# Kernel optimization log

Hardware: AMD Instinct MI355X
Metric: run time of the kernel (lower is better)

Reference implementation:

```python
import jax, jax.numpy as jnp
import numpy as np

B = 8; H = 128; W = 128; C = 256
NH = 16; HD = 16          # head_dim hard-coded to 16 in source
WS = 8; SS = 4            # window size / shift size
HID = 1024                # mlp hidden = 4 * C
SCALE = HD ** (-0.5)


def _rel_pos_index(ws):
    # same construction as torch buffer relative_position_index
    coords = np.stack(np.meshgrid(np.arange(ws), np.arange(ws), indexing='ij')).reshape(2, -1)
    rel = (coords[:, :, None] - coords[:, None, :]).transpose(1, 2, 0).copy()
    rel[..., 0] += ws - 1
    rel[..., 1] += ws - 1
    rel[..., 0] *= 2 * ws - 1
    return rel.sum(-1)  # (N, N) ints


def _attn_mask(h, w, ws, ss):
    # shifted-window mask, matches calculate_mask()
    img = np.zeros((h, w))
    sl = (slice(0, -ws), slice(-ws, -ss), slice(-ss, None))
    c = 0
    for hs in sl:
        for wsl in sl:
            img[hs, wsl] = c
            c += 1
    mw = img.reshape(h // ws, ws, w // ws, ws).transpose(0, 2, 1, 3).reshape(-1, ws * ws)
    d = mw[:, None, :] - mw[:, :, None]  # (nW, N, N)
    return np.where(d == 0, 0.0, -100.0).astype(np.float32)


def _ln(x, g, b, eps=1e-5):
    m = x.mean(-1, keepdims=True)
    v = ((x - m) ** 2).mean(-1, keepdims=True)
    return (x - m) * jax.lax.rsqrt(v + eps) * g + b


def setup_inputs() -> dict:
    key = jax.random.key(0)
    ks = jax.random.split(key, 12)
    inner = NH * HD
    std = 0.02
    return {
        'x': jax.random.normal(ks[0], (B, H * W, C), jnp.float32),
        'ln1_g': jnp.ones((C,), jnp.float32),
        'ln1_b': jnp.zeros((C,), jnp.float32),
        'q_w': jax.random.normal(ks[1], (C, inner), jnp.float32) * std,
        'q_b': jnp.zeros((inner,), jnp.float32),
        'k_w': jax.random.normal(ks[2], (C, inner), jnp.float32) * std,
        'k_b': jnp.zeros((inner,), jnp.float32),
        'v_w': jax.random.normal(ks[3], (C, inner), jnp.float32) * std,
        'v_b': jnp.zeros((inner,), jnp.float32),
        'rpb': jax.random.normal(ks[4], ((2 * WS - 1) * (2 * WS - 1), NH), jnp.float32) * std,
        'proj_w': jax.random.normal(ks[5], (inner, C), jnp.float32) * std,
        'proj_b': jnp.zeros((C,), jnp.float32),
        'ln2_g': jnp.ones((C,), jnp.float32),
        'ln2_b': jnp.zeros((C,), jnp.float32),
        'fc1_w': jax.random.normal(ks[6], (C, HID), jnp.float32) * std,
        'fc1_b': jnp.zeros((HID,), jnp.float32),
        'fc2_w': jax.random.normal(ks[7], (HID, C), jnp.float32) * std,
        'fc2_b': jnp.zeros((C,), jnp.float32),
        'H_in': 128,
        'W_in': 128,
    }


def reference(x, ln1_g, ln1_b, q_w, q_b, k_w, k_b, v_w, v_b, rpb,
              proj_w, proj_b, ln2_g, ln2_b, fc1_w, fc1_b, fc2_w, fc2_b,
              H_in, W_in):
    N = WS * WS
    nW = (H // WS) * (W // WS)
    idx = _rel_pos_index(WS)                       # static int (N, N)
    mask = jnp.asarray(_attn_mask(H, W, WS, SS))   # (nW, N, N)

    shortcut = x
    h = _ln(x, ln1_g, ln1_b).reshape(B, H, W, C)
    h = jnp.roll(h, (-SS, -SS), axis=(1, 2))
    # window partition -> (B*nW, N, C)
    h = h.reshape(B, H // WS, WS, W // WS, WS, C).transpose(0, 1, 3, 2, 4, 5)
    h = h.reshape(B * nW, N, C)

    q = (h @ q_w + q_b).reshape(-1, N, NH, HD).transpose(0, 2, 1, 3) * SCALE
    k = (h @ k_w + k_b).reshape(-1, N, NH, HD).transpose(0, 2, 1, 3)
    v = (h @ v_w + v_b).reshape(-1, N, NH, HD).transpose(0, 2, 1, 3)

    attn = jnp.einsum('bhnd,bhmd->bhnm', q, k)     # (B*nW, NH, N, N)
    bias = rpb[idx.reshape(-1)].reshape(N, N, NH).transpose(2, 0, 1)
    attn = attn + bias[None]
    attn = attn.reshape(B, nW, NH, N, N) + mask[None, :, None]
    attn = jax.nn.softmax(attn.reshape(B * nW, NH, N, N), axis=-1)

    o = jnp.einsum('bhnm,bhmd->bhnd', attn, v)
    o = o.transpose(0, 2, 1, 3).reshape(B * nW, N, NH * HD)
    o = o @ proj_w + proj_b

    # window reverse + roll back
    o = o.reshape(B, H // WS, W // WS, WS, WS, C).transpose(0, 1, 3, 2, 4, 5)
    o = o.reshape(B, H, W, C)
    o = jnp.roll(o, (SS, SS), axis=(1, 2)).reshape(B, H * W, C)

    x = shortcut + o
    h2 = _ln(x, ln2_g, ln2_b)
    h2 = jax.nn.gelu(h2 @ fc1_w + fc1_b, approximate=False)
    return x + (h2 @ fc2_w + fc2_b)
```

## Files before the change

### kernel.cpp

```cpp
#include <hip/hip_runtime.h>
#include <hip/hip_bf16.h>
#include <stdint.h>


#define SLOT ((size_t)64 << 20)

typedef __attribute__((ext_vector_type(8))) short bf16x8;
typedef __attribute__((ext_vector_type(4))) float f32x4;

union FU { float f; unsigned u; };

__device__ inline float bflo(unsigned p) { FU x; x.u = p << 16; return x.f; }
__device__ inline float bfhi(unsigned p) { FU x; x.u = p & 0xffff0000u; return x.f; }
__device__ inline unsigned short f2bf(float f) {
  FU x; x.f = f;
  unsigned r = x.u + 0x7fff + ((x.u >> 16) & 1);
  return (unsigned short)(r >> 16);
}
__device__ inline unsigned packbf2(float a, float b) {
  FU x, y; x.f = a; y.f = b;
  unsigned ra = (x.u + 0x7fff + ((x.u >> 16) & 1)) >> 16;
  unsigned rb = (y.u + 0x7fff + ((y.u >> 16) & 1)) & 0xffff0000u;
  return ra | rb;
}

__device__ inline float fast_gelu(float v) {
  return v / (1.0f + __expf(-1.702f * v));
}

__device__ inline void gload16(const void* g, void* l) {
  __builtin_amdgcn_global_load_lds(
      (const __attribute__((address_space(1))) unsigned int*)g,
      (__attribute__((address_space(3))) unsigned int*)l, 16, 0, 0);
}


__global__ __launch_bounds__(256) void build_qkvw(
    const float* __restrict__ qw, const float* __restrict__ kw, const float* __restrict__ vw,
    const float* __restrict__ qb, const float* __restrict__ kb, const float* __restrict__ vb,
    unsigned short* __restrict__ wt, float* __restrict__ bias) {
  int i = blockIdx.x * 256 + threadIdx.x;
  if (i < 768 * 256) {
    int n = i >> 8, c = i & 255;
    const float* w = (n < 256) ? qw : (n < 512 ? kw : vw);
    const float sc = (n < 256) ? 0.25f : 1.0f;
    int nn = n & 255;
    wt[i] = f2bf(sc * w[c * 256 + nn]);
  }
  if (i < 768) {
    bias[i] = (i < 256) ? 0.25f * qb[i] : (i < 512 ? kb[i - 256] : vb[i - 512]);
  }
}

__global__ __launch_bounds__(256) void wconv_t(
    const float* __restrict__ src, unsigned short* __restrict__ dst, int R, int C) {
  int i = blockIdx.x * 256 + threadIdx.x;
  if (i >= R * C) return;
  int n = i / R, c = i - n * R;
  dst[i] = f2bf(src[(size_t)c * C + n]);
}

__global__ __launch_bounds__(256) void ln1_roll_win(
    const float* __restrict__ x, const float* __restrict__ g, const float* __restrict__ b,
    unsigned short* __restrict__ hwin) {
  const int tok = blockIdx.x * 4 + (threadIdx.x >> 6);
  const int l = threadIdx.x & 63;
  const int n = tok & 63, wi = (tok >> 6) & 255, bb = tok >> 14;
  const int wh = wi >> 4, ww = wi & 15, r = n >> 3, c = n & 7;
  const int hs = (wh * 8 + r + 4) & 127;
  const int wsx = (ww * 8 + c + 4) & 127;
  const float* xr = x + ((size_t)bb * 16384 + hs * 128 + wsx) * 256;
  float4 v = *(const float4*)(xr + l * 4);
  float s = v.x + v.y + v.z + v.w;
#pragma unroll
  for (int off = 32; off; off >>= 1) s += __shfl_xor(s, off);
  const float mean = s * (1.f / 256.f);
  const float d0 = v.x - mean, d1 = v.y - mean, d2 = v.z - mean, d3 = v.w - mean;
  float vv = d0 * d0 + d1 * d1 + d2 * d2 + d3 * d3;
#pragma unroll
  for (int off = 32; off; off >>= 1) vv += __shfl_xor(vv, off);
  const float rs = rsqrtf(vv * (1.f / 256.f) + 1e-5f);
  float4 gg = *(const float4*)(g + l * 4);
  float4 bv = *(const float4*)(b + l * 4);
  uint2 outv;
  outv.x = packbf2(d0 * rs * gg.x + bv.x, d1 * rs * gg.y + bv.y);
  outv.y = packbf2(d2 * rs * gg.z + bv.z, d3 * rs * gg.w + bv.w);
  *(uint2*)(hwin + (size_t)tok * 256 + l * 4) = outv;
}

template <int EPI, int K, int N, int NBX>
__global__ __launch_bounds__(256) void gemm128(
    const unsigned short* __restrict__ A, const unsigned short* __restrict__ Bt,
    const float* __restrict__ bias, unsigned short* __restrict__ Cb,
    float* __restrict__ Cf) {
  __shared__ __align__(16) unsigned short smem[2][2][128 * 64];
  const int nwg = gridDim.x;
  const int q = nwg >> 3;
  const int swz = (blockIdx.x & 7) * q + (blockIdx.x >> 3);
  const int m0 = (swz / NBX) * 128;
  const int n0 = (swz % NBX) * 128;

  const int t = threadIdx.x, w = t >> 6, l = t & 63;
  const int lg = l >> 4, lm = l & 15;
  const int wr = w >> 1, wc = w & 1;

  const int srow = w * 32 + (l >> 3);
  const int scol = ((l & 7) ^ (l >> 3)) * 8;
  const unsigned short* Ap = A + (size_t)(m0 + srow) * K + scol;
  const unsigned short* Bp = Bt + (size_t)(n0 + srow) * K + scol;

  const int cb = n0 + wc * 64 + lm;
  f32x4 acc[4][4];
#pragma unroll
  for (int n = 0; n < 4; ++n) {
    const float bv = bias[cb + n * 16];
#pragma unroll
    for (int m = 0; m < 4; ++m) acc[m][n] = (f32x4){bv, bv, bv, bv};
  }

  constexpr int NT = K >> 6;
  const int cx = lg ^ (lm & 7);

#pragma unroll
  for (int i = 0; i < 4; ++i) {
    gload16(Ap + (size_t)(i * 8) * K, &smem[0][0][(w * 32 + i * 8) * 64]);
    gload16(Bp + (size_t)(i * 8) * K, &smem[0][1][(w * 32 + i * 8) * 64]);
  }
  __syncthreads();

#pragma unroll
  for (int kt = 0; kt < NT; ++kt) {
    const int cur = kt & 1;
    if (kt + 1 < NT) {
      const int ko = (kt + 1) << 6;
#pragma unroll
      for (int i = 0; i < 4; ++i) {
        gload16(Ap + (size_t)(i * 8) * K + ko, &smem[cur ^ 1][0][(w * 32 + i * 8) * 64]);
        gload16(Bp + (size_t)(i * 8) * K + ko, &smem[cur ^ 1][1][(w * 32 + i * 8) * 64]);
      }
    }
#pragma unroll
    for (int kk = 0; kk < 64; kk += 32) {
      const int ch = (cx ^ (kk >> 3)) * 8;
      bf16x8 af[4], bfr[4];
#pragma unroll
      for (int m = 0; m < 4; ++m)
        af[m] = *(const bf16x8*)&smem[cur][0][(wr * 64 + m * 16 + lm) * 64 + ch];
#pragma unroll
      for (int n = 0; n < 4; ++n)
        bfr[n] = *(const bf16x8*)&smem[cur][1][(wc * 64 + n * 16 + lm) * 64 + ch];
#pragma unroll
      for (int m = 0; m < 4; ++m)
#pragma unroll
        for (int n = 0; n < 4; ++n)
          acc[m][n] = __builtin_amdgcn_mfma_f32_16x16x32_bf16(af[m], bfr[n], acc[m][n], 0, 0, 0);
    }
    if (kt + 1 < NT) __syncthreads();
  }

  __syncthreads();
  float* Lp = (float*)smem;
#pragma unroll
  for (int m = 0; m < 4; ++m) {
#pragma unroll
    for (int n = 0; n < 4; ++n) {
      const int col = wc * 64 + n * 16 + lm;
#pragma unroll
      for (int r = 0; r < 4; ++r) {
        const int row = wr * 64 + m * 16 + lg * 4 + r;
        Lp[row * 128 + (col ^ (lg << 4))] = acc[m][n][r];
      }
    }
  }
  __syncthreads();
  const int rr0 = w * 32 + (l >> 5);
  const int cg = (l & 31) * 4;
#pragma unroll
  for (int p = 0; p < 16; ++p) {
    const int row = rr0 + p * 2;
    const int sc = cg ^ (((row >> 2) & 3) << 4);
    float4 v = *(const float4*)&Lp[row * 128 + sc];
    if (EPI == 2) {
      v.x = fast_gelu(v.x); v.y = fast_gelu(v.y);
      v.z = fast_gelu(v.z); v.w = fast_gelu(v.w);
    }
    if (EPI == 3) {
      float4* op = (float4*)&Cf[(size_t)(m0 + row) * N + n0 + cg];
      float4 o = *op;
      o.x += v.x; o.y += v.y; o.z += v.z; o.w += v.w;
      *op = o;
    } else {
      uint2 pk;
      pk.x = packbf2(v.x, v.y);
      pk.y = packbf2(v.z, v.w);
      *(uint2*)&Cb[(size_t)(m0 + row) * N + n0 + cg] = pk;
    }
  }
}

__global__ __launch_bounds__(256) void attn_mfma(
    const unsigned short* __restrict__ qkv, const float* __restrict__ rpb,
    unsigned short* __restrict__ o) {
  __shared__ float rps[16][226];
  __shared__ __align__(16) unsigned short Pl[4][64][72];
  const int win = blockIdx.x;
  const int wh = (win >> 4) & 15, ww = win & 15;
  const int t = threadIdx.x, wv = t >> 6, l = t & 63;
  const int lg = l >> 4, lm = l & 15;
  const unsigned short* base = qkv + (size_t)win * 64 * 768;

  for (int i = t; i < 3600; i += 256) rps[i & 15][i >> 4] = rpb[i];
  __syncthreads();

  const bool eH = (wh == 15), eW = (ww == 15);
  const bool edge = eH || eW;

  int qv[4], liq[4];
#pragma unroll
  for (int nt = 0; nt < 4; ++nt) {
    const int qn = nt * 16 + lm, ri = qn >> 3, ci = qn & 7;
    qv[nt] = ri * 15 + ci;
    liq[nt] = (eH ? (ri < 4 ? 1 : 2) : 0) * 3 + (eW ? (ci < 4 ? 1 : 2) : 0);
  }
  int kv[4][4], ljk[4][4];
#pragma unroll
  for (int mt = 0; mt < 4; ++mt)
#pragma unroll
    for (int r = 0; r < 4; ++r) {
      const int kn = mt * 16 + 4 * lg + r, rj = kn >> 3, cj = kn & 7;
      kv[mt][r] = rj * 15 + cj;
      ljk[mt][r] = (eH ? (rj < 4 ? 1 : 2) : 0) * 3 + (eW ? (cj < 4 ? 1 : 2) : 0);
    }

  const bf16x8 zf = {0, 0, 0, 0, 0, 0, 0, 0};

#pragma unroll 1
  for (int hi = 0; hi < 4; ++hi) {
    const int h = wv * 4 + hi;
    bf16x8 kf[4], qf[4];
#pragma unroll
    for (int i = 0; i < 4; ++i) {
      kf[i] = (lg < 2)
          ? *(const bf16x8*)(base + (size_t)(i * 16 + lm) * 768 + 256 + h * 16 + lg * 8)
          : zf;
      qf[i] = (lg < 2)
          ? *(const bf16x8*)(base + (size_t)(i * 16 + lm) * 768 + h * 16 + lg * 8)
          : zf;
    }
    f32x4 acc[4][4];
#pragma unroll
    for (int mt = 0; mt < 4; ++mt)
#pragma unroll
      for (int nt = 0; nt < 4; ++nt)
        acc[mt][nt] = (f32x4){0.f, 0.f, 0.f, 0.f};
#pragma unroll
    for (int mt = 0; mt < 4; ++mt)
#pragma unroll
      for (int nt = 0; nt < 4; ++nt)
        acc[mt][nt] = __builtin_amdgcn_mfma_f32_16x16x32_bf16(kf[mt], qf[nt], acc[mt][nt], 0, 0, 0);

#pragma unroll
    for (int nt = 0; nt < 4; ++nt) {
      float mx = -1e30f;
#pragma unroll
      for (int mt = 0; mt < 4; ++mt)
#pragma unroll
        for (int r = 0; r < 4; ++r) {
          float s = acc[mt][nt][r] + rps[h][qv[nt] - kv[mt][r] + 112];
          if (edge) s += (liq[nt] == ljk[mt][r]) ? 0.f : -100.f;
          acc[mt][nt][r] = s;
          mx = fmaxf(mx, s);
        }
      mx = fmaxf(mx, __shfl_xor(mx, 16));
      mx = fmaxf(mx, __shfl_xor(mx, 32));
      float sum = 0.f;
#pragma unroll
      for (int mt = 0; mt < 4; ++mt)
#pragma unroll
        for (int r = 0; r < 4; ++r) {
          const float p = __expf(acc[mt][nt][r] - mx);
          acc[mt][nt][r] = p;
          sum += p;
        }
      sum += __shfl_xor(sum, 16);
      sum += __shfl_xor(sum, 32);
      const float inv = 1.f / sum;
      const int qn = nt * 16 + lm;
#pragma unroll
      for (int mt = 0; mt < 4; ++mt) {
        uint2 pk;
        pk.x = packbf2(acc[mt][nt][0] * inv, acc[mt][nt][1] * inv);
        pk.y = packbf2(acc[mt][nt][2] * inv, acc[mt][nt][3] * inv);
        *(uint2*)&Pl[wv][qn][mt * 16 + 4 * lg] = pk;
      }
    }

    f32x4 oacc[4];
#pragma unroll
    for (int mt = 0; mt < 4; ++mt) oacc[mt] = (f32x4){0.f, 0.f, 0.f, 0.f};
#pragma unroll
    for (int kk = 0; kk < 2; ++kk) {
      bf16x8 vf;
#pragma unroll
      for (int j = 0; j < 8; ++j)
        vf[j] = (short)base[(size_t)(kk * 32 + lg * 8 + j) * 768 + 512 + h * 16 + lm];
#pragma unroll
      for (int mt = 0; mt < 4; ++mt) {
        bf16x8 pf = *(const bf16x8*)&Pl[wv][mt * 16 + lm][kk * 32 + lg * 8];
        oacc[mt] = __builtin_amdgcn_mfma_f32_16x16x32_bf16(pf, vf, oacc[mt], 0, 0, 0);
      }
    }
#pragma unroll
    for (int mt = 0; mt < 4; ++mt)
#pragma unroll
      for (int r = 0; r < 4; ++r)
        o[((size_t)win * 64 + mt * 16 + 4 * lg + r) * 256 + h * 16 + lm] = f2bf(oacc[mt][r]);
  }
}

__global__ __launch_bounds__(256) void scatter_ln2(
    const float* __restrict__ x, const unsigned short* __restrict__ po,
    const float* __restrict__ g, const float* __restrict__ b,
    float* __restrict__ x2, unsigned short* __restrict__ h2) {
  const int tok = blockIdx.x * 4 + (threadIdx.x >> 6);
  const int l = threadIdx.x & 63;
  const int bb = tok >> 14, pix = tok & 16383, hy = pix >> 7, wx = pix & 127;
  const int hr = (hy + 124) & 127, wc = (wx + 124) & 127;
  const int src = ((bb << 8) + (hr >> 3) * 16 + (wc >> 3)) * 64 + (hr & 7) * 8 + (wc & 7);
  float4 xv = *(const float4*)(x + (size_t)tok * 256 + l * 4);
  uint2 pv = *(const uint2*)(po + (size_t)src * 256 + l * 4);
  const float y0 = xv.x + bflo(pv.x);
  const float y1 = xv.y + bfhi(pv.x);
  const float y2 = xv.z + bflo(pv.y);
  const float y3 = xv.w + bfhi(pv.y);
  *(float4*)(x2 + (size_t)tok * 256 + l * 4) = make_float4(y0, y1, y2, y3);
  float s = y0 + y1 + y2 + y3;
#pragma unroll
  for (int off = 32; off; off >>= 1) s += __shfl_xor(s, off);
  const float mean = s * (1.f / 256.f);
  const float d0 = y0 - mean, d1 = y1 - mean, d2 = y2 - mean, d3 = y3 - mean;
  float vv = d0 * d0 + d1 * d1 + d2 * d2 + d3 * d3;
#pragma unroll
  for (int off = 32; off; off >>= 1) vv += __shfl_xor(vv, off);
  const float rs = rsqrtf(vv * (1.f / 256.f) + 1e-5f);
  float4 gg = *(const float4*)(g + l * 4);
  float4 bv = *(const float4*)(b + l * 4);
  uint2 outv;
  outv.x = packbf2(d0 * rs * gg.x + bv.x, d1 * rs * gg.y + bv.y);
  outv.y = packbf2(d2 * rs * gg.z + bv.z, d3 * rs * gg.w + bv.w);
  *(uint2*)(h2 + (size_t)tok * 256 + l * 4) = outv;
}


extern "C" void kernel_launch(void* const* d_in, const int* in_sizes, int n_in,
                              void* d_out, int out_size, void* d_ws, size_t ws_size,
                              hipStream_t stream) {
  const float* x = (const float*)d_in[0];
  const float* ln1g = (const float*)d_in[1];
  const float* ln1b = (const float*)d_in[2];
  const float* qw = (const float*)d_in[3];
  const float* qb = (const float*)d_in[4];
  const float* kw = (const float*)d_in[5];
  const float* kb = (const float*)d_in[6];
  const float* vw = (const float*)d_in[7];
  const float* vb = (const float*)d_in[8];
  const float* rpb = (const float*)d_in[9];
  const float* pw = (const float*)d_in[10];
  const float* pb = (const float*)d_in[11];
  const float* ln2g = (const float*)d_in[12];
  const float* ln2b = (const float*)d_in[13];
  const float* f1w = (const float*)d_in[14];
  const float* f1b = (const float*)d_in[15];
  const float* f2w = (const float*)d_in[16];
  const float* f2b = (const float*)d_in[17];
  float* out = (float*)d_out;

  char* wsb = (char*)d_ws;
  unsigned short* hwin = (unsigned short*)(wsb);
  unsigned short* qkv = (unsigned short*)(wsb + SLOT);
  unsigned short* po = (unsigned short*)(wsb + 4 * SLOT);
  unsigned short* g1 = qkv;
  unsigned short* wqkvt = (unsigned short*)(wsb + 5 * SLOT);
  unsigned short* projt = wqkvt + 768 * 256;
  unsigned short* fc1t = projt + 256 * 256;
  unsigned short* fc2t = fc1t + 1024 * 256;
  float* bqkv = (float*)(fc2t + 256 * 1024);

  build_qkvw<<<768, 256, 0, stream>>>(qw, kw, vw, qb, kb, vb, wqkvt, bqkv);
  wconv_t<<<256, 256, 0, stream>>>(pw, projt, 256, 256);
  wconv_t<<<1024, 256, 0, stream>>>(f1w, fc1t, 256, 1024);
  wconv_t<<<1024, 256, 0, stream>>>(f2w, fc2t, 1024, 256);

  ln1_roll_win<<<32768, 256, 0, stream>>>(x, ln1g, ln1b, hwin);
  gemm128<0, 256, 768, 6><<<6 * 1024, 256, 0, stream>>>(hwin, wqkvt, bqkv, qkv, nullptr);
  attn_mfma<<<2048, 256, 0, stream>>>(qkv, rpb, hwin);
  gemm128<0, 256, 256, 2><<<2 * 1024, 256, 0, stream>>>(hwin, projt, pb, po, nullptr);
  scatter_ln2<<<32768, 256, 0, stream>>>(x, po, ln2g, ln2b, out, hwin);
  gemm128<2, 256, 1024, 8><<<8 * 1024, 256, 0, stream>>>(hwin, fc1t, f1b, g1, nullptr);
  gemm128<3, 1024, 256, 2><<<2 * 1024, 256, 0, stream>>>(g1, fc2t, f2b, nullptr, out);
}
```

Before: 688.1 us.

## Fuse MLP fc1, GELU and fc2 into a single kernel keeping hidden tile in LDS

```diff
diff --git a/kernel.cpp b/kernel.cpp
--- a/kernel.cpp
+++ b/kernel.cpp
@@ -180,21 +180,134 @@
     const int row = rr0 + p * 2;
     const int sc = cg ^ (((row >> 2) & 3) << 4);
     float4 v = *(const float4*)&Lp[row * 128 + sc];
-    if (EPI == 2) {
-      v.x = fast_gelu(v.x); v.y = fast_gelu(v.y);
-      v.z = fast_gelu(v.z); v.w = fast_gelu(v.w);
-    }
-    if (EPI == 3) {
-      float4* op = (float4*)&Cf[(size_t)(m0 + row) * N + n0 + cg];
-      float4 o = *op;
-      o.x += v.x; o.y += v.y; o.z += v.z; o.w += v.w;
-      *op = o;
-    } else {
-      uint2 pk;
-      pk.x = packbf2(v.x, v.y);
-      pk.y = packbf2(v.z, v.w);
-      *(uint2*)&Cb[(size_t)(m0 + row) * N + n0 + cg] = pk;
-    }
+    uint2 pk;
+    pk.x = packbf2(v.x, v.y);
+    pk.y = packbf2(v.z, v.w);
+    *(uint2*)&Cb[(size_t)(m0 + row) * N + n0 + cg] = pk;
+  }
+}
+
+__global__ __launch_bounds__(256, 2) void fused_mlp(
+    const unsigned short* __restrict__ h2, const unsigned short* __restrict__ w1t,
+    const float* __restrict__ b1, const unsigned short* __restrict__ w2t,
+    const float* __restrict__ b2, float* __restrict__ out) {
+  __shared__ __align__(16) unsigned short smem[2 * 64 * 256];
+  unsigned short* As = smem;
+  unsigned short* Hs = smem + 64 * 256;
+  const int nwg = gridDim.x;
+  const int q = nwg >> 3;
+  const int swz = (blockIdx.x & 7) * q + (blockIdx.x >> 3);
+  const int m0 = swz * 64;
+
+  const int t = threadIdx.x, w = t >> 6, l = t & 63;
+  const int lg = l >> 4, lm = l & 15;
+
+#pragma unroll
+  for (int i = 0; i < 8; ++i) {
+    const int row = w * 16 + i * 2 + (l >> 5);
+    const int c = (l & 31) ^ (row & 7);
+    gload16(h2 + (size_t)(m0 + row) * 256 + c * 8, &As[(w * 16 + i * 2) * 256]);
+  }
+
+  f32x4 oacc[4][4];
+#pragma unroll
+  for (int n = 0; n < 4; ++n) {
+    const float bv = b2[w * 64 + n * 16 + lm];
+#pragma unroll
+    for (int m = 0; m < 4; ++m) oacc[m][n] = (f32x4){bv, bv, bv, bv};
+  }
+  __syncthreads();
+
+  for (int hc = 0; hc < 4; ++hc) {
+    if (hc) __syncthreads();
+#pragma unroll
+    for (int half = 0; half < 2; ++half) {
+      f32x4 a1[4][2];
+#pragma unroll
+      for (int n = 0; n < 2; ++n) {
+        const float bv = b1[hc * 256 + w * 64 + half * 32 + n * 16 + lm];
+#pragma unroll
+        for (int m = 0; m < 4; ++m) a1[m][n] = (f32x4){bv, bv, bv, bv};
+      }
+#pragma unroll
+      for (int kk = 0; kk < 8; ++kk) {
+        bf16x8 af[4], bw[2];
+#pragma unroll
+        for (int m = 0; m < 4; ++m) {
+          const int row = m * 16 + lm;
+          af[m] = *(const bf16x8*)((const char*)As + row * 512 +
+                                   ((kk * 64 + lg * 16) ^ ((row & 7) << 4)));
+        }
+#pragma unroll
+        for (int n = 0; n < 2; ++n)
+          bw[n] = *(const bf16x8*)(w1t +
+                   (size_t)(hc * 256 + w * 64 + half * 32 + n * 16 + lm) * 256 +
+                   kk * 32 + lg * 8);
+#pragma unroll
+        for (int m = 0; m < 4; ++m)
+#pragma unroll
+          for (int n = 0; n < 2; ++n)
+            a1[m][n] = __builtin_amdgcn_mfma_f32_16x16x32_bf16(af[m], bw[n], a1[m][n], 0, 0, 0);
+      }
+#pragma unroll
+      for (int m = 0; m < 4; ++m)
+#pragma unroll
+        for (int n = 0; n < 2; ++n)
+#pragma unroll
+          for (int r = 0; r < 4; ++r) {
+            const int hrow = m * 16 + lg * 4 + r;
+            const int hcol = w * 64 + half * 32 + n * 16 + lm;
+            *(unsigned short*)((char*)Hs + hrow * 512 +
+                               ((hcol * 2) ^ ((hrow & 7) << 4))) = f2bf(fast_gelu(a1[m][n][r]));
+          }
+    }
+    __syncthreads();
+#pragma unroll
+    for (int ks = 0; ks < 8; ++ks) {
+      bf16x8 hf[4], bw2[4];
+#pragma unroll
+      for (int m = 0; m < 4; ++m) {
+        const int row = m * 16 + lm;
+        hf[m] = *(const bf16x8*)((const char*)Hs + row * 512 +
+                                 ((ks * 64 + lg * 16) ^ ((row & 7) << 4)));
+      }
+#pragma unroll
+      for (int n = 0; n < 4; ++n)
+        bw2[n] = *(const bf16x8*)(w2t + (size_t)(w * 64 + n * 16 + lm) * 1024 +
+                                  hc * 256 + ks * 32 + lg * 8);
+#pragma unroll
+      for (int m = 0; m < 4; ++m)
+#pragma unroll
+        for (int n = 0; n < 4; ++n)
+          oacc[m][n] = __builtin_amdgcn_mfma_f32_16x16x32_bf16(hf[m], bw2[n], oacc[m][n], 0, 0, 0);
+    }
+  }
+
+  __syncthreads();
+  float* Lf = (float*)smem;
+#pragma unroll
+  for (int m = 0; m < 4; ++m)
+#pragma unroll
+    for (int n = 0; n < 4; ++n) {
+      const int col = w * 64 + n * 16 + lm;
+#pragma unroll
+      for (int r = 0; r < 4; ++r) {
+        const int row = m * 16 + lg * 4 + r;
+        Lf[row * 256 + (col ^ (lg << 4))] = oacc[m][n][r];
+      }
+    }
+  __syncthreads();
+#pragma unroll
+  for (int p = 0; p < 16; ++p) {
+    const int fidx = p * 256 + t;
+    const int row = fidx >> 6;
+    const int c4 = (fidx & 63) * 4;
+    const int c4r = c4 ^ (((row >> 2) & 3) << 4);
+    float4 v = *(const float4*)&Lf[row * 256 + c4r];
+    float4* op = (float4*)&out[(size_t)(m0 + row) * 256 + c4];
+    float4 o = *op;
+    o.x += v.x; o.y += v.y; o.z += v.z; o.w += v.w;
+    *op = o;
   }
 }
 
@@ -379,7 +492,6 @@
   unsigned short* hwin = (unsigned short*)(wsb);
   unsigned short* qkv = (unsigned short*)(wsb + SLOT);
   unsigned short* po = (unsigned short*)(wsb + 4 * SLOT);
-  unsigned short* g1 = qkv;
   unsigned short* wqkvt = (unsigned short*)(wsb + 5 * SLOT);
   unsigned short* projt = wqkvt + 768 * 256;
   unsigned short* fc1t = projt + 256 * 256;
@@ -396,6 +508,5 @@
   attn_mfma<<<2048, 256, 0, stream>>>(qkv, rpb, hwin);
   gemm128<0, 256, 256, 2><<<2 * 1024, 256, 0, stream>>>(hwin, projt, pb, po, nullptr);
   scatter_ln2<<<32768, 256, 0, stream>>>(x, po, ln2g, ln2b, out, hwin);
-  gemm128<2, 256, 1024, 8><<<8 * 1024, 256, 0, stream>>>(hwin, fc1t, f1b, g1, nullptr);
-  gemm128<3, 1024, 256, 2><<<2 * 1024, 256, 0, stream>>>(g1, fc2t, f2b, nullptr, out);
-}
+  fused_mlp<<<2048, 256, 0, stream>>>(hwin, fc1t, f1b, fc2t, f2b, out);
+}
```

Measured after the change: 695.2 us. Within noise of the previous version (+1.0%).

## Halve GEMM K-tile to 32 and split epilogue staging into two halves

Applied to the files above, without the earlier changes.

```diff
diff --git a/kernel.cpp b/kernel.cpp
--- a/kernel.cpp
+++ b/kernel.cpp
@@ -93,7 +93,7 @@
     const unsigned short* __restrict__ A, const unsigned short* __restrict__ Bt,
     const float* __restrict__ bias, unsigned short* __restrict__ Cb,
     float* __restrict__ Cf) {
-  __shared__ __align__(16) unsigned short smem[2][2][128 * 64];
+  __shared__ __align__(16) unsigned short smem[2][2][128 * 32];
   const int nwg = gridDim.x;
   const int q = nwg >> 3;
   const int swz = (blockIdx.x & 7) * q + (blockIdx.x >> 3);
@@ -104,27 +104,27 @@
   const int lg = l >> 4, lm = l & 15;
   const int wr = w >> 1, wc = w & 1;
 
-  const int srow = w * 32 + (l >> 3);
-  const int scol = ((l & 7) ^ (l >> 3)) * 8;
+  const int srow = w * 32 + (l >> 2);
+  const int scol = ((l & 3) ^ ((l >> 2) & 3)) * 8;
   const unsigned short* Ap = A + (size_t)(m0 + srow) * K + scol;
   const unsigned short* Bp = Bt + (size_t)(n0 + srow) * K + scol;
 
-  const int cb = n0 + wc * 64 + lm;
+  const int cbs = n0 + wc * 64 + lm;
   f32x4 acc[4][4];
 #pragma unroll
   for (int n = 0; n < 4; ++n) {
-    const float bv = bias[cb + n * 16];
+    const float bv = bias[cbs + n * 16];
 #pragma unroll
     for (int m = 0; m < 4; ++m) acc[m][n] = (f32x4){bv, bv, bv, bv};
   }
 
-  constexpr int NT = K >> 6;
-  const int cx = lg ^ (lm & 7);
-
-#pragma unroll
-  for (int i = 0; i < 4; ++i) {
-    gload16(Ap + (size_t)(i * 8) * K, &smem[0][0][(w * 32 + i * 8) * 64]);
-    gload16(Bp + (size_t)(i * 8) * K, &smem[0][1][(w * 32 + i * 8) * 64]);
+  constexpr int NT = K >> 5;
+  const int chA = (lg ^ (lm & 3)) * 8;
+
+#pragma unroll
+  for (int i = 0; i < 2; ++i) {
+    gload16(Ap + (size_t)(i * 16) * K, &smem[0][0][(w * 32 + i * 16) * 32]);
+    gload16(Bp + (size_t)(i * 16) * K, &smem[0][1][(w * 32 + i * 16) * 32]);
   }
   __syncthreads();
 
@@ -132,68 +132,69 @@
   for (int kt = 0; kt < NT; ++kt) {
     const int cur = kt & 1;
     if (kt + 1 < NT) {
-      const int ko = (kt + 1) << 6;
-#pragma unroll
-      for (int i = 0; i < 4; ++i) {
-        gload16(Ap + (size_t)(i * 8) * K + ko, &smem[cur ^ 1][0][(w * 32 + i * 8) * 64]);
-        gload16(Bp + (size_t)(i * 8) * K + ko, &smem[cur ^ 1][1][(w * 32 + i * 8) * 64]);
+      const int ko = (kt + 1) << 5;
+#pragma unroll
+      for (int i = 0; i < 2; ++i) {
+        gload16(Ap + (size_t)(i * 16) * K + ko, &smem[cur ^ 1][0][(w * 32 + i * 16) * 32]);
+        gload16(Bp + (size_t)(i * 16) * K + ko, &smem[cur ^ 1][1][(w * 32 + i * 16) * 32]);
       }
     }
-#pragma unroll
-    for (int kk = 0; kk < 64; kk += 32) {
-      const int ch = (cx ^ (kk >> 3)) * 8;
-      bf16x8 af[4], bfr[4];
+    bf16x8 af[4], bfr[4];
+#pragma unroll
+    for (int m = 0; m < 4; ++m)
+      af[m] = *(const bf16x8*)&smem[cur][0][(wr * 64 + m * 16 + lm) * 32 + chA];
+#pragma unroll
+    for (int n = 0; n < 4; ++n)
+      bfr[n] = *(const bf16x8*)&smem[cur][1][(wc * 64 + n * 16 + lm) * 32 + chA];
+#pragma unroll
+    for (int m = 0; m < 4; ++m)
+#pragma unroll
+      for (int n = 0; n < 4; ++n)
+        acc[m][n] = __builtin_amdgcn_mfma_f32_16x16x32_bf16(af[m], bfr[n], acc[m][n], 0, 0, 0);
+    if (kt + 1 < NT) __syncthreads();
+  }
+
+  float* Lp = (float*)smem;
+#pragma unroll
+  for (int h = 0; h < 2; ++h) {
+    __syncthreads();
+    if (wr == h) {
 #pragma unroll
       for (int m = 0; m < 4; ++m)
-        af[m] = *(const bf16x8*)&smem[cur][0][(wr * 64 + m * 16 + lm) * 64 + ch];
-#pragma unroll
-      for (int n = 0; n < 4; ++n)
-        bfr[n] = *(const bf16x8*)&smem[cur][1][(wc * 64 + n * 16 + lm) * 64 + ch];
-#pragma unroll
-      for (int m = 0; m < 4; ++m)
-#pragma unroll
-        for (int n = 0; n < 4; ++n)
-          acc[m][n] = __builtin_amdgcn_mfma_f32_16x16x32_bf16(af[m], bfr[n], acc[m][n], 0, 0, 0);
-    }
-    if (kt + 1 < NT) __syncthreads();
-  }
-
-  __syncthreads();
-  float* Lp = (float*)smem;
-#pragma unroll
-  for (int m = 0; m < 4; ++m) {
-#pragma unroll
-    for (int n = 0; n < 4; ++n) {
-      const int col = wc * 64 + n * 16 + lm;
-#pragma unroll
-      for (int r = 0; r < 4; ++r) {
-        const int row = wr * 64 + m * 16 + lg * 4 + r;
-        Lp[row * 128 + (col ^ (lg << 4))] = acc[m][n][r];
+#pragma unroll
+        for (int n = 0; n < 4; ++n) {
+          const int col = wc * 64 + n * 16 + lm;
+#pragma unroll
+          for (int r = 0; r < 4; ++r) {
+            const int rowl = m * 16 + lg * 4 + r;
+            Lp[rowl * 128 + (col ^ (lg << 4))] = acc[m][n][r];
+          }
+        }
+    }
+    __syncthreads();
+#pragma unroll
+    for (int p = 0; p < 8; ++p) {
+      const int fidx = p * 256 + t;
+      const int rowl = fidx >> 5;
+      const int c4 = (fidx & 31) * 4;
+      const int sc = c4 ^ (((rowl >> 2) & 3) << 4);
+      float4 v = *(const float4*)&Lp[rowl * 128 + sc];
+      const int grow = m0 + h * 64 + rowl;
+      if (EPI == 2) {
+        v.x = fast_gelu(v.x); v.y = fast_gelu(v.y);
+        v.z = fast_gelu(v.z); v.w = fast_gelu(v.w);
       }
-    }
-  }
-  __syncthreads();
-  const int rr0 = w * 32 + (l >> 5);
-  const int cg = (l & 31) * 4;
-#pragma unroll
-  for (int p = 0; p < 16; ++p) {
-    const int row = rr0 + p * 2;
-    const int sc = cg ^ (((row >> 2) & 3) << 4);
-    float4 v = *(const float4*)&Lp[row * 128 + sc];
-    if (EPI == 2) {
-      v.x = fast_gelu(v.x); v.y = fast_gelu(v.y);
-      v.z = fast_gelu(v.z); v.w = fast_gelu(v.w);
-    }
-    if (EPI == 3) {
-      float4* op = (float4*)&Cf[(size_t)(m0 + row) * N + n0 + cg];
-      float4 o = *op;
-      o.x += v.x; o.y += v.y; o.z += v.z; o.w += v.w;
-      *op = o;
-    } else {
-      uint2 pk;
-      pk.x = packbf2(v.x, v.y);
-      pk.y = packbf2(v.z, v.w);
-      *(uint2*)&Cb[(size_t)(m0 + row) * N + n0 + cg] = pk;
+      if (EPI == 3) {
+        float4* op = (float4*)&Cf[(size_t)grow * N + n0 + c4];
+        float4 o = *op;
+        o.x += v.x; o.y += v.y; o.z += v.z; o.w += v.w;
+        *op = o;
+      } else {
+        uint2 pk;
+        pk.x = packbf2(v.x, v.y);
+        pk.y = packbf2(v.z, v.w);
+        *(uint2*)&Cb[(size_t)grow * N + n0 + c4] = pk;
+      }
     }
   }
 }
```

New measurement: 727.5 us. 5.7% more time.

## Enlarge GEMM tiles to 256x256 with 512-thread workgroups

Applied to the files above, without the earlier changes.

```diff
diff --git a/kernel.cpp b/kernel.cpp
--- a/kernel.cpp
+++ b/kernel.cpp
@@ -89,33 +89,32 @@
 }
 
 template <int EPI, int K, int N, int NBX>
-__global__ __launch_bounds__(256) void gemm128(
+__global__ __launch_bounds__(512, 2) void gemm256(
     const unsigned short* __restrict__ A, const unsigned short* __restrict__ Bt,
     const float* __restrict__ bias, unsigned short* __restrict__ Cb,
     float* __restrict__ Cf) {
-  __shared__ __align__(16) unsigned short smem[2][2][128 * 64];
+  __shared__ __align__(16) unsigned short smem[2][2][256 * 64];
   const int nwg = gridDim.x;
   const int q = nwg >> 3;
   const int swz = (blockIdx.x & 7) * q + (blockIdx.x >> 3);
-  const int m0 = (swz / NBX) * 128;
-  const int n0 = (swz % NBX) * 128;
+  const int m0 = (swz / NBX) * 256;
+  const int n0 = (swz % NBX) * 256;
 
   const int t = threadIdx.x, w = t >> 6, l = t & 63;
   const int lg = l >> 4, lm = l & 15;
-  const int wr = w >> 1, wc = w & 1;
-
-  const int srow = w * 32 + (l >> 3);
+  const int wr = w >> 2, wn = w & 3;
+
+  const int srow = w * 8 + (l >> 3);
   const int scol = ((l & 7) ^ (l >> 3)) * 8;
   const unsigned short* Ap = A + (size_t)(m0 + srow) * K + scol;
   const unsigned short* Bp = Bt + (size_t)(n0 + srow) * K + scol;
 
-  const int cb = n0 + wc * 64 + lm;
-  f32x4 acc[4][4];
+  f32x4 acc[8][4];
 #pragma unroll
   for (int n = 0; n < 4; ++n) {
-    const float bv = bias[cb + n * 16];
-#pragma unroll
-    for (int m = 0; m < 4; ++m) acc[m][n] = (f32x4){bv, bv, bv, bv};
+    const float bv = bias[n0 + wn * 64 + n * 16 + lm];
+#pragma unroll
+    for (int m = 0; m < 8; ++m) acc[m][n] = (f32x4){bv, bv, bv, bv};
   }
 
   constexpr int NT = K >> 6;
@@ -123,8 +122,8 @@
 
 #pragma unroll
   for (int i = 0; i < 4; ++i) {
-    gload16(Ap + (size_t)(i * 8) * K, &smem[0][0][(w * 32 + i * 8) * 64]);
-    gload16(Bp + (size_t)(i * 8) * K, &smem[0][1][(w * 32 + i * 8) * 64]);
+    gload16(Ap + (size_t)(i * 64) * K, &smem[0][0][(i * 64 + w * 8) * 64]);
+    gload16(Bp + (size_t)(i * 64) * K, &smem[0][1][(i * 64 + w * 8) * 64]);
   }
   __syncthreads();
 
@@ -135,22 +134,22 @@
       const int ko = (kt + 1) << 6;
 #pragma unroll
       for (int i = 0; i < 4; ++i) {
-        gload16(Ap + (size_t)(i * 8) * K + ko, &smem[cur ^ 1][0][(w * 32 + i * 8) * 64]);
-        gload16(Bp + (size_t)(i * 8) * K + ko, &smem[cur ^ 1][1][(w * 32 + i * 8) * 64]);
+        gload16(Ap + (size_t)(i * 64) * K + ko, &smem[cur ^ 1][0][(i * 64 + w * 8) * 64]);
+        gload16(Bp + (size_t)(i * 64) * K + ko, &smem[cur ^ 1][1][(i * 64 + w * 8) * 64]);
       }
     }
 #pragma unroll
     for (int kk = 0; kk < 64; kk += 32) {
       const int ch = (cx ^ (kk >> 3)) * 8;
-      bf16x8 af[4], bfr[4];
-#pragma unroll
-      for (int m = 0; m < 4; ++m)
-        af[m] = *(const bf16x8*)&smem[cur][0][(wr * 64 + m * 16 + lm) * 64 + ch];
+      bf16x8 af[8], bfr[4];
+#pragma unroll
+      for (int m = 0; m < 8; ++m)
+        af[m] = *(const bf16x8*)&smem[cur][0][(wr * 128 + m * 16 + lm) * 64 + ch];
 #pragma unroll
       for (int n = 0; n < 4; ++n)
-        bfr[n] = *(const bf16x8*)&smem[cur][1][(wc * 64 + n * 16 + lm) * 64 + ch];
-#pragma unroll
-      for (int m = 0; m < 4; ++m)
+        bfr[n] = *(const bf16x8*)&smem[cur][1][(wn * 64 + n * 16 + lm) * 64 + ch];
+#pragma unroll
+      for (int m = 0; m < 8; ++m)
 #pragma unroll
         for (int n = 0; n < 4; ++n)
           acc[m][n] = __builtin_amdgcn_mfma_f32_16x16x32_bf16(af[m], bfr[n], acc[m][n], 0, 0, 0);
@@ -158,42 +157,47 @@
     if (kt + 1 < NT) __syncthreads();
   }
 
-  __syncthreads();
   float* Lp = (float*)smem;
 #pragma unroll
-  for (int m = 0; m < 4; ++m) {
-#pragma unroll
-    for (int n = 0; n < 4; ++n) {
-      const int col = wc * 64 + n * 16 + lm;
-#pragma unroll
-      for (int r = 0; r < 4; ++r) {
-        const int row = wr * 64 + m * 16 + lg * 4 + r;
-        Lp[row * 128 + (col ^ (lg << 4))] = acc[m][n][r];
+  for (int h = 0; h < 2; ++h) {
+    __syncthreads();
+    if (wr == h) {
+#pragma unroll
+      for (int m = 0; m < 8; ++m)
+#pragma unroll
+        for (int n = 0; n < 4; ++n) {
+          const int col = wn * 64 + n * 16 + lm;
+#pragma unroll
+          for (int r = 0; r < 4; ++r) {
+            const int rowl = m * 16 + lg * 4 + r;
+            Lp[rowl * 256 + (col ^ (lg << 4))] = acc[m][n][r];
+          }
+        }
+    }
+    __syncthreads();
+#pragma unroll
+    for (int p = 0; p < 16; ++p) {
+      const int fidx = p * 512 + t;
+      const int rowl = fidx >> 6;
+      const int c4 = (fidx & 63) * 4;
+      const int sc = c4 ^ (((rowl >> 2) & 3) << 4);
+      float4 v = *(const float4*)&Lp[rowl * 256 + sc];
+      const int grow = m0 + h * 128 + rowl;
+      if (EPI == 2) {
+        v.x = fast_gelu(v.x); v.y = fast_gelu(v.y);
+        v.z = fast_gelu(v.z); v.w = fast_gelu(v.w);
       }
-    }
-  }
-  __syncthreads();
-  const int rr0 = w * 32 + (l >> 5);
-  const int cg = (l & 31) * 4;
-#pragma unroll
-  for (int p = 0; p < 16; ++p) {
-    const int row = rr0 + p * 2;
-    const int sc = cg ^ (((row >> 2) & 3) << 4);
-    float4 v = *(const float4*)&Lp[row * 128 + sc];
-    if (EPI == 2) {
-      v.x = fast_gelu(v.x); v.y = fast_gelu(v.y);
-      v.z = fast_gelu(v.z); v.w = fast_gelu(v.w);
-    }
-    if (EPI == 3) {
-      float4* op = (float4*)&Cf[(size_t)(m0 + row) * N + n0 + cg];
-      float4 o = *op;
-      o.x += v.x; o.y += v.y; o.z += v.z; o.w += v.w;
-      *op = o;
-    } else {
-      uint2 pk;
-      pk.x = packbf2(v.x, v.y);
-      pk.y = packbf2(v.z, v.w);
-      *(uint2*)&Cb[(size_t)(m0 + row) * N + n0 + cg] = pk;
+      if (EPI == 3) {
+        float4* op = (float4*)&Cf[(size_t)grow * N + n0 + c4];
+        float4 o = *op;
+        o.x += v.x; o.y += v.y; o.z += v.z; o.w += v.w;
+        *op = o;
+      } else {
+        uint2 pk;
+        pk.x = packbf2(v.x, v.y);
+        pk.y = packbf2(v.z, v.w);
+        *(uint2*)&Cb[(size_t)grow * N + n0 + c4] = pk;
+      }
     }
   }
 }
@@ -392,10 +396,10 @@
   wconv_t<<<1024, 256, 0, stream>>>(f2w, fc2t, 1024, 256);
 
   ln1_roll_win<<<32768, 256, 0, stream>>>(x, ln1g, ln1b, hwin);
-  gemm128<0, 256, 768, 6><<<6 * 1024, 256, 0, stream>>>(hwin, wqkvt, bqkv, qkv, nullptr);
+  gemm256<0, 256, 768, 3><<<512 * 3, 512, 0, stream>>>(hwin, wqkvt, bqkv, qkv, nullptr);
   attn_mfma<<<2048, 256, 0, stream>>>(qkv, rpb, hwin);
-  gemm128<0, 256, 256, 2><<<2 * 1024, 256, 0, stream>>>(hwin, projt, pb, po, nullptr);
+  gemm256<0, 256, 256, 1><<<512, 512, 0, stream>>>(hwin, projt, pb, po, nullptr);
   scatter_ln2<<<32768, 256, 0, stream>>>(x, po, ln2g, ln2b, out, hwin);
-  gemm128<2, 256, 1024, 8><<<8 * 1024, 256, 0, stream>>>(hwin, fc1t, f1b, g1, nullptr);
-  gemm128<3, 1024, 256, 2><<<2 * 1024, 256, 0, stream>>>(g1, fc2t, f2b, nullptr, out);
-}
+  gemm256<2, 256, 1024, 4><<<512 * 4, 512, 0, stream>>>(hwin, fc1t, f1b, g1, nullptr);
+  gemm256<3, 1024, 256, 1><<<512, 512, 0, stream>>>(g1, fc2t, f2b, nullptr, out);
+}
```

Measured after the change: 822.9 us. 19.6% more time.
